# Kernel tuning notes

Measured on AMD Instinct MI355X. Metric: run time of the kernel, lower is better.

Reference implementation:

```python
import jax, jax.numpy as jnp
import numpy as np

N, B, T, D, H = 200, 100, 256, 5, 20  # count_lstms, batch, seq_len, io units, lstm units


def setup_inputs() -> dict:
    key = jax.random.key(0)
    ks = jax.random.split(key, 4)
    inputs = jax.random.normal(ks[0], (B, T, D), dtype=jnp.float32)
    # Stacked per-LSTM parameters (Keras gate order: i, f, c, o)
    W = jax.random.normal(ks[1], (N, D, 4 * H), dtype=jnp.float32) * (1.0 / np.sqrt(D))
    U = jax.random.normal(ks[2], (N, H, 4 * H), dtype=jnp.float32) * (1.0 / np.sqrt(H))
    b = jnp.zeros((N, 4 * H), dtype=jnp.float32)
    dense_W = jax.random.normal(ks[3], (N * H, D), dtype=jnp.float32) * (1.0 / np.sqrt(N * H))
    dense_b = jnp.zeros((D,), dtype=jnp.float32)
    return {"inputs": inputs, "W": W, "U": U, "b": b, "dense_W": dense_W, "dense_b": dense_b}


def reference(inputs, W, U, b, dense_W, dense_b):
    # inputs: [B, T, D]; W: [N, D, 4H]; U: [N, H, 4H]; b: [N, 4H]
    n, h = W.shape[0], U.shape[1]
    batch = inputs.shape[0]
    x_t = jnp.transpose(inputs, (1, 0, 2))  # [T, B, D]
    h0 = jnp.zeros((n, batch, h), dtype=inputs.dtype)
    c0 = jnp.zeros((n, batch, h), dtype=inputs.dtype)

    def step(carry, xt):
        hprev, cprev = carry
        # gates for all N lstms at once: [N, B, 4H]
        z = (jnp.einsum('bd,ndk->nbk', xt, W)
             + jnp.einsum('nbh,nhk->nbk', hprev, U)
             + b[:, None, :])
        zi, zf, zg, zo = jnp.split(z, 4, axis=-1)
        i = jax.nn.sigmoid(zi)
        f = jax.nn.sigmoid(zf)
        g = jnp.tanh(zg)
        o = jax.nn.sigmoid(zo)
        cnew = f * cprev + i * g
        hnew = o * jnp.tanh(cnew)
        return (hnew, cnew), hnew

    (_, _), hs = jax.lax.scan(step, (h0, c0), x_t)  # hs: [T, N, B, H]
    # concat along feature axis -> [B, T, N*H]
    concat = jnp.transpose(hs, (2, 0, 1, 3)).reshape(batch, x_t.shape[0], n * h)
    out = concat @ dense_W + dense_b  # [B, T, D]
    return out
```

## Files before the change

kernel.cpp:

```cpp
#include <hip/hip_runtime.h>
#include <math.h>

constexpr int NL = 200;
constexpr int B  = 100;
constexpr int T  = 256;
constexpr int D  = 5;
constexpr int H  = 20;
constexpr int NW = 7;
constexpr int KP = 40;
constexpr int NWAVE = 5;
constexpr int BLKT  = 64 * NWAVE;
constexpr int BPAD  = 112;
constexpr int NPAIR = NL / 2;

constexpr int KX = 24;

typedef float  f32x4  __attribute__((ext_vector_type(4)));
typedef short  bf16x8 __attribute__((ext_vector_type(8)));

__device__ __forceinline__ float rcpf(float x) { return __builtin_amdgcn_rcpf(x); }

#if __has_builtin(__builtin_amdgcn_exp2f)
__device__ __forceinline__ float exp2fast(float x) { return __builtin_amdgcn_exp2f(x); }
#else
__device__ __forceinline__ float exp2fast(float x) { return __expf(x * 0.6931471805599453f); }
#endif

__device__ __forceinline__ unsigned short f2bf(float f) {
    union { float f; unsigned u; } v; v.f = f;
    unsigned r = v.u + 0x7fffu + ((v.u >> 16) & 1u);
    return (unsigned short)(r >> 16);
}
__device__ __forceinline__ unsigned pk2bf(float lo, float hi) {
    return (unsigned)f2bf(lo) | ((unsigned)f2bf(hi) << 16);
}

__device__ __forceinline__ void block_sync_lds() {
    asm volatile("s_waitcnt lgkmcnt(0)" ::: "memory");
    __builtin_amdgcn_s_barrier();
}

constexpr float NLOG2E = -1.4426950408889634f;
constexpr float TLOG2E = 2.8853900817779268f;

__global__ __launch_bounds__(256) void init_out_kernel(const float* __restrict__ dense_b,
                                                       float* __restrict__ out, int n) {
    int i = blockIdx.x * 256 + threadIdx.x;
    if (i < n) out[i] = dense_b[i % D];
}

__global__ __launch_bounds__(256) void xpack_kernel(const float* __restrict__ x,
                                                    int4* __restrict__ xe) {
    int i = blockIdx.x * 256 + threadIdx.x;
    if (i >= T * BPAD) return;
    const int t = i / BPAD;
    const int b = i % BPAD;
    int4 v = {0, 0, 0, 0};
    if (b < B) {
        const float* s = x + ((size_t)b * T + t) * D;
        v.x = (int)pk2bf(s[0], s[1]);
        v.y = (int)pk2bf(s[2], s[3]);
        v.z = (int)pk2bf(s[4], 0.0f);
        v.w = 0x00003F80;
    }
    xe[i] = v;
}

__device__ __forceinline__ float lstm_act(const f32x4 a, float& c) {
    const float iv = rcpf(1.0f + exp2fast(a[0]));
    const float fv = rcpf(1.0f + exp2fast(a[1]));
    const float gv = fmaf(-2.0f, rcpf(exp2fast(a[2]) + 1.0f), 1.0f);
    const float ov = rcpf(1.0f + exp2fast(a[3]));
    c = fmaf(fv, c, iv * gv);
    const float th = fmaf(-2.0f, rcpf(exp2fast(TLOG2E * c) + 1.0f), 1.0f);
    return ov * th;
}

template<bool USE_WS>
__global__ __attribute__((amdgpu_flat_work_group_size(BLKT, BLKT)))
void lstm_mfma5x2_kernel(
    const int4*  __restrict__ xe,
    const float* __restrict__ Wg,
    const float* __restrict__ Ug,
    const float* __restrict__ bg,
    const float* __restrict__ dWg,
    float* __restrict__ pw,
    float* __restrict__ out)
{
    const int blk = blockIdx.x;
    const int pr  = blk / NW;
    const int w   = blk % NW;
    const int n0  = pr;
    const int n1  = pr + NPAIR;
    const int tid = threadIdx.x;
    const int wid = tid >> 6;
    const int l   = tid & 63;
    const int c16 = l & 15;
    const int g4  = l >> 4;

    __shared__ __align__(16) short bcol[2][2][16][KP];

    for (int i = tid; i < 2 * 2 * 16 * KP / 2; i += BLKT)
        ((int*)&bcol[0][0][0][0])[i] = 0;

    const int gateA = c16 & 3;
    const int hA4   = c16 >> 2;
    const float sA  = (gateA == 2) ? TLOG2E : NLOG2E;
    auto buildA = [&](int n) {
        const float* Un = Ug + (size_t)n * H * 4 * H;
        const float* Wn = Wg + (size_t)n * D * 4 * H;
        const float* bn = bg + (size_t)n * 4 * H;
        const int colA  = gateA * H + (wid * 4 + hA4);
        bf16x8 a;
        #pragma unroll
        for (int j = 0; j < 8; ++j) {
            const int k = 8 * g4 + j;
            float v = 0.0f;
            if (k < KX) {
                const int mt = k % 6, gg = k / 6;
                if (mt < 5) v = Un[(mt * 4 + gg) * 4 * H + colA];
            } else if (k < KX + D) {
                v = Wn[(k - KX) * 4 * H + colA];
            } else if (k == 30) {
                v = bn[colA];
            }
            a[j] = (short)f2bf(sA * v);
        }
        return a;
    };
    auto buildD = [&](int n) {
        const float* dn = dWg + (size_t)n * H * D;
        bf16x8 a;
        #pragma unroll
        for (int j = 0; j < 8; ++j) {
            const int k = 8 * g4 + j;
            float v = 0.0f;
            if (c16 < D && k < KX) {
                const int mt = k % 6, gg = k / 6;
                if (mt < 5) v = dn[(mt * 4 + gg) * D + c16];
            }
            a[j] = (short)f2bf(v);
        }
        return a;
    };
    const bf16x8 af0 = buildA(n0);
    const bf16x8 af1 = buildA(n1);
    bf16x8 afd0 = {}, afd1 = {};
    if (wid == 1) { afd0 = buildD(n0); afd1 = buildD(n1); }

    const int  bgl    = w * 16 + c16;
    const bool bvalid = bgl < B;
    const int4* xq = xe + bgl;
    float* pwn = USE_WS ? (pw + (size_t)pr * T * (D * B))
                        : (out + ((size_t)bgl * T) * D);

    __syncthreads();

    int4 xn4;
    if (wid == 0 && l < 16) {
        const int4 x0 = xq[0];
        *(int4*)&bcol[0][0][c16][KX] = x0;
        *(int4*)&bcol[1][0][c16][KX] = x0;
        xn4 = xq[(T > 1 ? 1 : 0) * BPAD];
    }
    __syncthreads();

    float cst0 = 0.0f, cst1 = 0.0f;
    const f32x4 zero4 = {0.0f, 0.0f, 0.0f, 0.0f};
    int p = 0;

    for (int t = 0; t < T; ++t) {
        const bf16x8 bf0 = *(const bf16x8*)&bcol[0][p][c16][8 * g4];
        const bf16x8 bf1 = *(const bf16x8*)&bcol[1][p][c16][8 * g4];

        if (wid == 1) {
            const f32x4 acc0 = __builtin_amdgcn_mfma_f32_16x16x32_bf16(
                afd0, bf0, zero4, 0, 0, 0);
            const f32x4 accd = __builtin_amdgcn_mfma_f32_16x16x32_bf16(
                afd1, bf1, acc0, 0, 0, 0);
            if (t > 0 && bvalid) {
                #pragma unroll
                for (int reg = 0; reg < 4; ++reg) {
                    const int d = g4 * 4 + reg;
                    if (d < D) {
                        if (USE_WS)
                            pwn[(size_t)(t - 1) * (D * B) + d * B + bgl] = accd[reg];
                        else
                            atomicAdd(&pwn[(size_t)(t - 1) * D + d], accd[reg]);
                    }
                }
            }
        }

        const f32x4 a0 = __builtin_amdgcn_mfma_f32_16x16x32_bf16(af0, bf0, zero4, 0, 0, 0);
        const f32x4 a1 = __builtin_amdgcn_mfma_f32_16x16x32_bf16(af1, bf1, zero4, 0, 0, 0);
        const float h0 = lstm_act(a0, cst0);
        const float h1 = lstm_act(a1, cst1);

        bcol[0][p ^ 1][c16][g4 * 6 + wid] = (short)f2bf(h0);
        bcol[1][p ^ 1][c16][g4 * 6 + wid] = (short)f2bf(h1);

        if (wid == 0 && l < 16) {
            *(int4*)&bcol[0][p ^ 1][c16][KX] = xn4;
            *(int4*)&bcol[1][p ^ 1][c16][KX] = xn4;
            const int tc = (t + 2 < T) ? t + 2 : T - 1;
            xn4 = xq[(size_t)tc * BPAD];
        }

        block_sync_lds();
        p ^= 1;
    }

    if (wid == 1) {
        const bf16x8 bf0 = *(const bf16x8*)&bcol[0][p][c16][8 * g4];
        const bf16x8 bf1 = *(const bf16x8*)&bcol[1][p][c16][8 * g4];
        const f32x4 acc0 = __builtin_amdgcn_mfma_f32_16x16x32_bf16(
            afd0, bf0, zero4, 0, 0, 0);
        const f32x4 accd = __builtin_amdgcn_mfma_f32_16x16x32_bf16(
            afd1, bf1, acc0, 0, 0, 0);
        if (bvalid) {
            #pragma unroll
            for (int reg = 0; reg < 4; ++reg) {
                const int d = g4 * 4 + reg;
                if (d < D) {
                    if (USE_WS)
                        pwn[(size_t)(T - 1) * (D * B) + d * B + bgl] = accd[reg];
                    else
                        atomicAdd(&pwn[(size_t)(T - 1) * D + d], accd[reg]);
                }
            }
        }
    }
}

__global__ __launch_bounds__(512) void reduce_kernel(
    const float* __restrict__ pw, const float* __restrict__ dense_b,
    float* __restrict__ out)
{
    const int t    = blockIdx.x;
    const int flat = threadIdx.x;
    if (flat >= B * D) return;
    const int d = flat / B;
    const int b = flat % B;
    const float* p = pw + (size_t)t * (D * B) + flat;
    constexpr size_t stride = (size_t)T * D * B;
    float a0 = 0.0f, a1 = 0.0f;
    #pragma unroll 10
    for (int n = 0; n < NPAIR; n += 2) {
        a0 += p[(size_t)n * stride];
        a1 += p[(size_t)(n + 1) * stride];
    }
    out[((size_t)b * T + t) * D + d] = a0 + a1 + dense_b[d];
}

extern "C" void kernel_launch(void* const* d_in, const int* in_sizes, int n_in,
                              void* d_out, int out_size, void* d_ws, size_t ws_size,
                              hipStream_t stream) {
    const float* x   = (const float*)d_in[0];
    const float* Wg  = (const float*)d_in[1];
    const float* Ug  = (const float*)d_in[2];
    const float* bg  = (const float*)d_in[3];
    const float* dWg = (const float*)d_in[4];
    const float* dbv = (const float*)d_in[5];
    float* out = (float*)d_out;

    const size_t xe_bytes = (size_t)T * BPAD * sizeof(int4);
    const size_t pw_bytes = (size_t)NPAIR * T * D * B * sizeof(float);

    int4* xe = (int4*)d_ws;
    xpack_kernel<<<(T * BPAD + 255) / 256, 256, 0, stream>>>(x, xe);

    if (ws_size >= xe_bytes + pw_bytes) {
        float* pw = (float*)((char*)d_ws + xe_bytes);
        lstm_mfma5x2_kernel<true><<<NPAIR * NW, BLKT, 0, stream>>>(xe, Wg, Ug, bg, dWg, pw, out);
        reduce_kernel<<<T, 512, 0, stream>>>(pw, dbv, out);
    } else {
        init_out_kernel<<<(out_size + 255) / 256, 256, 0, stream>>>(dbv, out, out_size);
        lstm_mfma5x2_kernel<false><<<NPAIR * NW, BLKT, 0, stream>>>(xe, Wg, Ug, bg, dWg, nullptr, out);
    }
}
```

Baseline: 198.6 us.

## Process four LSTMs per block instead of two to halve block count

Each workgroup now runs four independent LSTM recurrences (n, n+50, n+100, n+150) instead of two. The grid shrinks from 700 to 350 blocks, and the dense-projection MFMA work is split across waves 1 and 2, each writing its own pair slot in the workspace. The aim is to give each wave more independent MFMA and activation chains to interleave within the serial time loop and to reduce block scheduling overhead. In exchange it raises per-thread register and LDS use, and it adds a waves_per_eu hint that may limit occupancy.

Result: slower. 269.8 us (+35.8%).

```diff
diff --git a/kernel.cpp b/kernel.cpp
--- a/kernel.cpp
+++ b/kernel.cpp
@@ -11,6 +11,8 @@
 constexpr int NWAVE = 5;
 constexpr int BLKT  = 64 * NWAVE;
 constexpr int BPAD  = 112;
+constexpr int NJ = 4;
+constexpr int NQ = NL / NJ;
 constexpr int NPAIR = NL / 2;
 
 constexpr int KX = 24;
@@ -77,8 +79,9 @@
 }
 
 template<bool USE_WS>
-__global__ __attribute__((amdgpu_flat_work_group_size(BLKT, BLKT)))
-void lstm_mfma5x2_kernel(
+__global__ __attribute__((amdgpu_flat_work_group_size(BLKT, BLKT),
+                          amdgpu_waves_per_eu(1, 3)))
+void lstm_mfma5x4_kernel(
     const int4*  __restrict__ xe,
     const float* __restrict__ Wg,
     const float* __restrict__ Ug,
@@ -88,19 +91,17 @@
     float* __restrict__ out)
 {
     const int blk = blockIdx.x;
-    const int pr  = blk / NW;
+    const int qr  = blk / NW;
     const int w   = blk % NW;
-    const int n0  = pr;
-    const int n1  = pr + NPAIR;
     const int tid = threadIdx.x;
     const int wid = tid >> 6;
     const int l   = tid & 63;
     const int c16 = l & 15;
     const int g4  = l >> 4;
 
-    __shared__ __align__(16) short bcol[2][2][16][KP];
-
-    for (int i = tid; i < 2 * 2 * 16 * KP / 2; i += BLKT)
+    __shared__ __align__(16) short bcol[NJ][2][16][KP];
+
+    for (int i = tid; i < NJ * 2 * 16 * KP / 2; i += BLKT)
         ((int*)&bcol[0][0][0][0])[i] = 0;
 
     const int gateA = c16 & 3;
@@ -143,15 +144,19 @@
         }
         return a;
     };
-    const bf16x8 af0 = buildA(n0);
-    const bf16x8 af1 = buildA(n1);
-    bf16x8 afd0 = {}, afd1 = {};
-    if (wid == 1) { afd0 = buildD(n0); afd1 = buildD(n1); }
+    const bf16x8 af0 = buildA(qr);
+    const bf16x8 af1 = buildA(qr + NQ);
+    const bf16x8 af2 = buildA(qr + 2 * NQ);
+    const bf16x8 af3 = buildA(qr + 3 * NQ);
+    bf16x8 afdA = {}, afdB = {};
+    if (wid == 1)      { afdA = buildD(qr);          afdB = buildD(qr + NQ); }
+    else if (wid == 2) { afdA = buildD(qr + 2 * NQ); afdB = buildD(qr + 3 * NQ); }
 
     const int  bgl    = w * 16 + c16;
     const bool bvalid = bgl < B;
     const int4* xq = xe + bgl;
-    float* pwn = USE_WS ? (pw + (size_t)pr * T * (D * B))
+    const int pair = qr * 2 + (wid == 2 ? 1 : 0);
+    float* pwn = USE_WS ? (pw + (size_t)pair * T * (D * B))
                         : (out + ((size_t)bgl * T) * D);
 
     __syncthreads();
@@ -159,25 +164,29 @@
     int4 xn4;
     if (wid == 0 && l < 16) {
         const int4 x0 = xq[0];
-        *(int4*)&bcol[0][0][c16][KX] = x0;
-        *(int4*)&bcol[1][0][c16][KX] = x0;
+        #pragma unroll
+        for (int j = 0; j < NJ; ++j) *(int4*)&bcol[j][0][c16][KX] = x0;
         xn4 = xq[(T > 1 ? 1 : 0) * BPAD];
     }
     __syncthreads();
 
-    float cst0 = 0.0f, cst1 = 0.0f;
+    float cst0 = 0.0f, cst1 = 0.0f, cst2 = 0.0f, cst3 = 0.0f;
     const f32x4 zero4 = {0.0f, 0.0f, 0.0f, 0.0f};
     int p = 0;
 
     for (int t = 0; t < T; ++t) {
         const bf16x8 bf0 = *(const bf16x8*)&bcol[0][p][c16][8 * g4];
         const bf16x8 bf1 = *(const bf16x8*)&bcol[1][p][c16][8 * g4];
-
-        if (wid == 1) {
+        const bf16x8 bf2 = *(const bf16x8*)&bcol[2][p][c16][8 * g4];
+        const bf16x8 bf3 = *(const bf16x8*)&bcol[3][p][c16][8 * g4];
+
+        if (wid == 1 || wid == 2) {
+            const bf16x8 bA = (wid == 1) ? bf0 : bf2;
+            const bf16x8 bB = (wid == 1) ? bf1 : bf3;
             const f32x4 acc0 = __builtin_amdgcn_mfma_f32_16x16x32_bf16(
-                afd0, bf0, zero4, 0, 0, 0);
+                afdA, bA, zero4, 0, 0, 0);
             const f32x4 accd = __builtin_amdgcn_mfma_f32_16x16x32_bf16(
-                afd1, bf1, acc0, 0, 0, 0);
+                afdB, bB, acc0, 0, 0, 0);
             if (t > 0 && bvalid) {
                 #pragma unroll
                 for (int reg = 0; reg < 4; ++reg) {
@@ -194,15 +203,21 @@
 
         const f32x4 a0 = __builtin_amdgcn_mfma_f32_16x16x32_bf16(af0, bf0, zero4, 0, 0, 0);
         const f32x4 a1 = __builtin_amdgcn_mfma_f32_16x16x32_bf16(af1, bf1, zero4, 0, 0, 0);
+        const f32x4 a2 = __builtin_amdgcn_mfma_f32_16x16x32_bf16(af2, bf2, zero4, 0, 0, 0);
+        const f32x4 a3 = __builtin_amdgcn_mfma_f32_16x16x32_bf16(af3, bf3, zero4, 0, 0, 0);
         const float h0 = lstm_act(a0, cst0);
         const float h1 = lstm_act(a1, cst1);
+        const float h2 = lstm_act(a2, cst2);
+        const float h3 = lstm_act(a3, cst3);
 
         bcol[0][p ^ 1][c16][g4 * 6 + wid] = (short)f2bf(h0);
         bcol[1][p ^ 1][c16][g4 * 6 + wid] = (short)f2bf(h1);
+        bcol[2][p ^ 1][c16][g4 * 6 + wid] = (short)f2bf(h2);
+        bcol[3][p ^ 1][c16][g4 * 6 + wid] = (short)f2bf(h3);
 
         if (wid == 0 && l < 16) {
-            *(int4*)&bcol[0][p ^ 1][c16][KX] = xn4;
-            *(int4*)&bcol[1][p ^ 1][c16][KX] = xn4;
+            #pragma unroll
+            for (int j = 0; j < NJ; ++j) *(int4*)&bcol[j][p ^ 1][c16][KX] = xn4;
             const int tc = (t + 2 < T) ? t + 2 : T - 1;
             xn4 = xq[(size_t)tc * BPAD];
         }
@@ -211,13 +226,14 @@
         p ^= 1;
     }
 
-    if (wid == 1) {
-        const bf16x8 bf0 = *(const bf16x8*)&bcol[0][p][c16][8 * g4];
-        const bf16x8 bf1 = *(const bf16x8*)&bcol[1][p][c16][8 * g4];
+    if (wid == 1 || wid == 2) {
+        const int jA = (wid == 1) ? 0 : 2;
+        const bf16x8 bA = *(const bf16x8*)&bcol[jA][p][c16][8 * g4];
+        const bf16x8 bB = *(const bf16x8*)&bcol[jA + 1][p][c16][8 * g4];
         const f32x4 acc0 = __builtin_amdgcn_mfma_f32_16x16x32_bf16(
-            afd0, bf0, zero4, 0, 0, 0);
+            afdA, bA, zero4, 0, 0, 0);
         const f32x4 accd = __builtin_amdgcn_mfma_f32_16x16x32_bf16(
-            afd1, bf1, acc0, 0, 0, 0);
+            afdB, bB, acc0, 0, 0, 0);
         if (bvalid) {
             #pragma unroll
             for (int reg = 0; reg < 4; ++reg) {
@@ -272,10 +288,10 @@
 
     if (ws_size >= xe_bytes + pw_bytes) {
         float* pw = (float*)((char*)d_ws + xe_bytes);
-        lstm_mfma5x2_kernel<true><<<NPAIR * NW, BLKT, 0, stream>>>(xe, Wg, Ug, bg, dWg, pw, out);
+        lstm_mfma5x4_kernel<true><<<NQ * NW, BLKT, 0, stream>>>(xe, Wg, Ug, bg, dWg, pw, out);
         reduce_kernel<<<T, 512, 0, stream>>>(pw, dbv, out);
     } else {
         init_out_kernel<<<(out_size + 255) / 256, 256, 0, stream>>>(dbv, out, out_size);
-        lstm_mfma5x2_kernel<false><<<NPAIR * NW, BLKT, 0, stream>>>(xe, Wg, Ug, bg, dWg, nullptr, out);
-    }
-}
+        lstm_mfma5x4_kernel<false><<<NQ * NW, BLKT, 0, stream>>>(xe, Wg, Ug, bg, dWg, nullptr, out);
+    }
+}
```
